# Kernel optimization log

Measured on AMD Instinct MI355X. Metric: run time of the kernel, lower is better.

Reference implementation:

```python
import jax, jax.numpy as jnp
import numpy as np

NBINS = (128, 64, 32)
LOG2PI = float(np.log(2.0 * np.pi))


def _quadratic_spline_stack(x, genes_oi, local_gene_ix, delta, uh, uw):
    """Stack of piecewise-quadratic (piecewise-linear density) splines on [0,1].
    Per split with n heights / n-1 widths (n-1 bins). Returns (outputs, logabsdet)."""
    uh_oi = uh[genes_oi]  # [G, sum(n)]
    uw_oi = uw[genes_oi]  # [G, sum(n-1)]
    outputs = x
    logabsdet = jnp.zeros_like(x)
    oh = ow = od = 0
    for n in NBINS:
        nh, nw = n, n - 1
        uhs = uh_oi[:, oh:oh + nh]
        uws = uw_oi[:, ow:ow + nw]
        ds = delta[:, od:od + nh]
        oh += nh; ow += nw; od += nh
        # per-gene bin widths / locations
        widths_g = jax.nn.softmax(uws, axis=-1)                     # [G, nw]
        bl = jnp.cumsum(widths_g, axis=-1)
        bl = bl.at[:, -1].set(1.0)
        bin_loc_g = jnp.pad(bl, ((0, 0), (1, 0)))                   # [G, nw+1]
        # gather per cut
        w = widths_g[local_gene_ix]                                 # [N, nw]
        loc = bin_loc_g[local_gene_ix]                              # [N, nw+1]
        # per-cut knot heights: gene baseline + cell/gene delta, normalized to unit area
        h_un = jnp.exp(uhs[local_gene_ix] + ds)                     # [N, nh]
        area = jnp.sum(0.5 * (h_un[:, :-1] + h_un[:, 1:]) * w, axis=-1, keepdims=True)
        h = h_un / area                                             # [N, nh]
        seg = 0.5 * (h[:, :-1] + h[:, 1:]) * w                      # bin masses [N, nw]
        left_cdf = jnp.pad(jnp.cumsum(seg, axis=-1)[:, :-1], ((0, 0), (1, 0)))  # [N, nw]
        # locate bin
        bin_idx = jnp.clip(jnp.sum(outputs[:, None] >= loc, axis=-1) - 1, 0, nw - 1)
        gi = bin_idx[:, None]
        loc_l = jnp.take_along_axis(loc, gi, -1)[:, 0]
        w_b = jnp.take_along_axis(w, gi, -1)[:, 0]
        cdf_l = jnp.take_along_axis(left_cdf, gi, -1)[:, 0]
        h_l = jnp.take_along_axis(h, gi, -1)[:, 0]
        h_r = jnp.take_along_axis(h, gi + 1, -1)[:, 0]
        alpha = (outputs - loc_l) / w_b
        outputs = (0.5 * (h_r - h_l) * w_b) * alpha * alpha + h_l * w_b * alpha + cdf_l
        logabsdet = logabsdet + jnp.log(h_l + (h_r - h_l) * alpha)
    return outputs, logabsdet


def setup_inputs() -> dict:
    key = jax.random.key(0)
    ks = jax.random.split(key, 10)
    B, L, G_total, G_oi, C, N = 512, 16, 20000, 500, 224, 200000
    clustering = jax.random.uniform(ks[0], (B, L), dtype=jnp.float32)
    coordinates = jax.random.uniform(ks[1], (N,), dtype=jnp.float32, minval=1e-4, maxval=1.0 - 1e-4)
    genes_oi = jax.random.randint(ks[2], (G_oi,), 0, G_total)
    local_gene_ix = jax.random.randint(ks[3], (N,), 0, G_oi)
    local_cellxgene_ix = jax.random.randint(ks[4], (N,), 0, B * G_oi)
    localcellxgene_ix = jax.random.randint(ks[5], (N,), 0, B * G_total)
    logit_weight = jax.random.normal(ks[6], (G_total, L, C), dtype=jnp.float32) * 0.01
    rho_weight = jax.random.normal(ks[7], (G_total, L), dtype=jnp.float32) * 0.05
    rho_bias = 1e-5 + (1.0 - 1e-5) * jax.random.uniform(ks[8], (G_total,), dtype=jnp.float32)
    k9, k10 = jax.random.split(ks[9])
    unnormalized_heights = jax.random.normal(k9, (G_total, sum(NBINS)), dtype=jnp.float32) * 0.1
    unnormalized_widths = jax.random.normal(k10, (G_total, sum(n - 1 for n in NBINS)), dtype=jnp.float32) * 0.1
    return dict(clustering=clustering, coordinates=coordinates, genes_oi=genes_oi,
                local_gene_ix=local_gene_ix, local_cellxgene_ix=local_cellxgene_ix,
                localcellxgene_ix=localcellxgene_ix, logit_weight=logit_weight,
                rho_weight=rho_weight, rho_bias=rho_bias,
                unnormalized_heights=unnormalized_heights,
                unnormalized_widths=unnormalized_widths)


def reference(clustering, coordinates, genes_oi, local_gene_ix, local_cellxgene_ix,
              localcellxgene_ix, logit_weight, rho_weight, rho_bias,
              unnormalized_heights, unnormalized_widths):
    B = clustering.shape[0]
    G = genes_oi.shape[0]
    n_total_genes = rho_bias.shape[0]
    # Decoder (n_layers=0 -> nn_output = latent)
    lw_oi = logit_weight[genes_oi]                                   # [G, L, C]
    mixture_delta = jnp.einsum('bl,glc->bgc', clustering, lw_oi)     # [B, G, C]
    rho_delta = clustering @ rho_weight.T                            # [B, G_total]
    rho = jax.nn.softmax(jnp.log(rho_bias)[None, :] + rho_delta, axis=-1)
    rho_cuts = rho.reshape(-1)[localcellxgene_ix]                    # [N]
    md_cuts = mixture_delta.reshape(B * G, -1)[local_cellxgene_ix]   # [N, C]
    _, lik_mixture = _quadratic_spline_stack(coordinates, genes_oi, local_gene_ix,
                                             md_cuts, unnormalized_heights, unnormalized_widths)
    lik_overall = jnp.log(rho_cuts) + jnp.log(jnp.float32(n_total_genes))
    elbo = -jnp.sum(lik_mixture + lik_overall)
    # Normal(0, exp(log_scale=0)=1) regularization log-probs
    def normal_logpdf(v):
        return -0.5 * v * v - 0.5 * LOG2PI
    elbo = elbo - jnp.sum(normal_logpdf(lw_oi))
    elbo = elbo - jnp.sum(normal_logpdf(rho_weight[genes_oi]))
    return elbo
```

## Files before the change

kernel.cpp:

```cpp
#include <hip/hip_runtime.h>
#include <cstddef>

#define LOG2PI_F 1.8378770664093453f

typedef float f2 __attribute__((ext_vector_type(2)));

__device__ __forceinline__ float wave_sum(float v) {
#pragma unroll
    for (int o = 32; o >= 1; o >>= 1) v += __shfl_xor(v, o, 64);
    return v;
}
__device__ __forceinline__ float wave_max(float v) {
#pragma unroll
    for (int o = 32; o >= 1; o >>= 1) v = fmaxf(v, __shfl_xor(v, o, 64));
    return v;
}
__device__ __forceinline__ float wave_scan_incl(float v, int lane) {
#pragma unroll
    for (int o = 1; o < 64; o <<= 1) {
        float t = __shfl_up(v, o, 64);
        if (lane >= o) v += t;
    }
    return v;
}

__device__ __forceinline__ float dot16(const f2* __restrict__ a, const f2* __restrict__ b) {
    f2 dv = a[0] * b[0];
#pragma unroll
    for (int l = 1; l < 8; ++l) dv = __builtin_elementwise_fma(a[l], b[l], dv);
    return dv.x + dv.y;
}

__global__ void k_prep_genes(const int* __restrict__ genes_oi,
                             const float* __restrict__ uh, const float* __restrict__ uw,
                             float4* __restrict__ pk, int* __restrict__ counts, int G_oi) {
    const int g = blockIdx.x;
    const int t = threadIdx.x;
    if (t == 0) counts[g] = 0;
    const int gs = genes_oi[g];
    const float* uhg = uh + (size_t)gs * 224;
    const float* uwg = uw + (size_t)gs * 221;

    const int NH[3] = {128, 64, 32};
    const int OH[3] = {0, 128, 192};
    const int OW[3] = {0, 127, 190};
    const int SO[3] = {0, 128, 191};
#pragma unroll
    for (int lev = 0; lev < 3; ++lev) {
        const int nw = NH[lev] - 1;
        float v0 = (t < nw)      ? uwg[OW[lev] + t]      : -INFINITY;
        float v1 = (t + 64 < nw) ? uwg[OW[lev] + t + 64] : -INFINITY;
        float mx = wave_max(fmaxf(v0, v1));
        float e0 = (t < nw)      ? __expf(v0 - mx) : 0.f;
        float e1 = (t + 64 < nw) ? __expf(v1 - mx) : 0.f;
        float inv = 1.0f / wave_sum(e0 + e1);
        float w0 = e0 * inv, w1 = e1 * inv;
        float i0 = wave_scan_incl(w0, t);
        float tot0 = __shfl(i0, 63, 64);
        float i1 = wave_scan_incl(w1, t) + tot0;
        if (t < nw) {
            float loc = (t == nw - 1) ? 1.0f : i0;
            pk[(size_t)(SO[lev] + t) * G_oi + g] = make_float4(uhg[OH[lev] + t + 1], 0.5f * w0, loc, 0.f);
        }
        if (t + 64 < nw) {
            int j = t + 64;
            float loc = (j == nw - 1) ? 1.0f : i1;
            pk[(size_t)(SO[lev] + j) * G_oi + g] = make_float4(uhg[OH[lev] + j + 1], 0.5f * w1, loc, 0.f);
        }
    }
    if (t == 0) pk[(size_t)127 * G_oi + g] = make_float4(uhg[0], uhg[128], uhg[192], 0.f);
}

__global__ void k_prep_lwT(const int* __restrict__ genes_oi,
                           const float* __restrict__ lw, const float* __restrict__ rw,
                           float* __restrict__ lwT, float* __restrict__ pB) {
    const int g = blockIdx.x;
    const int tid = threadIdx.x;
    const int gs = genes_oi[g];
    const float* src = lw + (size_t)gs * 3584;
    float* dst = lwT + (size_t)g * 3584;
    float acc = 0.f;
    if (tid < 224) {
        float vv[16];
#pragma unroll
        for (int l = 0; l < 16; ++l) {
            float v = src[l * 224 + tid];
            vv[l] = v;
            acc = fmaf(v, v, acc);
        }
        float4* d4 = (float4*)(dst + (size_t)tid * 16);
#pragma unroll
        for (int q = 0; q < 4; ++q)
            d4[q] = make_float4(vv[4 * q + 0], vv[4 * q + 1], vv[4 * q + 2], vv[4 * q + 3]);
    }
    if (tid < 16) { float v = rw[(size_t)gs * 16 + tid]; acc = fmaf(v, v, acc); }
    __shared__ float sm[256];
    sm[tid] = acc;
    __syncthreads();
    for (int o = 128; o > 0; o >>= 1) { if (tid < o) sm[tid] += sm[tid + o]; __syncthreads(); }
    if (tid == 0) pB[g] = 0.5f * sm[0] + 0.5f * LOG2PI_F * (3584.0f + 16.0f);
}

__global__ void k_hist_logrb(const int* __restrict__ lcx, int* __restrict__ counts,
                             const float* __restrict__ rho_bias, float* __restrict__ logrb,
                             int N, int G_oi, int G_total) {
    int i = blockIdx.x * blockDim.x + threadIdx.x;
    if (i < G_total) logrb[i] = __logf(rho_bias[i]);
    if (i < N) atomicAdd(&counts[(unsigned)lcx[i] % (unsigned)G_oi], 1);
}

__global__ void k_scan(const int* __restrict__ counts, int* __restrict__ offsets,
                       int* __restrict__ cursor, int G_oi) {
    __shared__ int sm[512];
    const int t = threadIdx.x;
    int v = (t < G_oi) ? counts[t] : 0;
    sm[t] = v;
    __syncthreads();
    for (int o = 1; o < 512; o <<= 1) {
        int add = (t >= o) ? sm[t - o] : 0;
        __syncthreads();
        sm[t] += add;
        __syncthreads();
    }
    if (t < G_oi) {
        offsets[t + 1] = sm[t];
        cursor[t] = sm[t] - v;
    }
    if (t == 0) offsets[0] = 0;
}

__global__ void k_scatter(const float* __restrict__ coord, const int* __restrict__ lgix,
                          const int* __restrict__ lcx, const int* __restrict__ lc2,
                          int* __restrict__ cursor, float4* __restrict__ xv, int N, int G_oi) {
    int i = blockIdx.x * blockDim.x + threadIdx.x;
    if (i >= N) return;
    unsigned v = (unsigned)lcx[i];
    unsigned g = v % (unsigned)G_oi;
    int pos = atomicAdd(&cursor[g], 1);
    int b1 = (int)(v / (unsigned)G_oi);
    xv[pos] = make_float4(coord[i], __int_as_float((b1 << 16) | lgix[i]),
                          __int_as_float(lc2[i]), 0.f);
}

__global__ void k_lse4(const float* __restrict__ clustering, const float* __restrict__ rw,
                       const float* __restrict__ logrb, float* __restrict__ lse,
                       int G_total, int B) {
    const int b0 = blockIdx.x * 4;
    const int tid = threadIdx.x;
    const int nc = min(4, B - b0);

    f2 cl[4][8];
#pragma unroll
    for (int c = 0; c < 4; ++c) {
        if (c < nc) {
            const float4* c4 = (const float4*)(clustering + (size_t)(b0 + c) * 16);
#pragma unroll
            for (int q = 0; q < 4; ++q) {
                float4 v = c4[q];
                cl[c][2 * q + 0] = (f2){v.x, v.y};
                cl[c][2 * q + 1] = (f2){v.z, v.w};
            }
        } else {
#pragma unroll
            for (int l = 0; l < 8; ++l) cl[c][l] = (f2){0.f, 0.f};
        }
    }

    float m[4], s[4];
#pragma unroll
    for (int c = 0; c < 4; ++c) { m[c] = -INFINITY; s[c] = 0.f; }

    for (int g = tid; g < G_total; g += 256) {
        const float4* r4 = (const float4*)(rw + (size_t)g * 16);
        f2 rv[8];
#pragma unroll
        for (int q = 0; q < 4; ++q) {
            float4 v = r4[q];
            rv[2 * q + 0] = (f2){v.x, v.y};
            rv[2 * q + 1] = (f2){v.z, v.w};
        }
        const float lb = logrb[g];
#pragma unroll
        for (int c = 0; c < 4; ++c) {
            float d = dot16(cl[c], rv);
            float logit = lb + d;
            float mn = fmaxf(m[c], logit);
            s[c] = s[c] * __expf(m[c] - mn) + __expf(logit - mn);
            m[c] = mn;
        }
    }

    __shared__ float ms[4][256], ss[4][256];
#pragma unroll
    for (int c = 0; c < 4; ++c) { ms[c][tid] = m[c]; ss[c][tid] = s[c]; }
    __syncthreads();
    for (int o = 128; o > 0; o >>= 1) {
        if (tid < o) {
#pragma unroll
            for (int c = 0; c < 4; ++c) {
                float m2 = ms[c][tid + o], s2 = ss[c][tid + o];
                float mn = fmaxf(ms[c][tid], m2);
                ss[c][tid] = ss[c][tid] * __expf(ms[c][tid] - mn) + s2 * __expf(m2 - mn);
                ms[c][tid] = mn;
            }
        }
        __syncthreads();
    }
    if (tid < 4 && tid < nc) lse[b0 + tid] = ms[tid][0] + __logf(ss[tid][0]);
}

__launch_bounds__(512, 4)
__global__ void k_main2(const float4* __restrict__ xv,
                        const int* __restrict__ offsets,
                        const float* __restrict__ clustering,
                        const float* __restrict__ lwT,
                        const float4* __restrict__ pk,
                        const float* __restrict__ rw,
                        const float* __restrict__ logrb,
                        const float* __restrict__ lse,
                        float* __restrict__ pA, int G_oi, int G_total) {
    const int g = blockIdx.x;
    const int tid = threadIdx.x;
    const float* lwg = lwT + (size_t)g * 3584;
    const int s = offsets[g], e = offsets[g + 1];
    const float logGt = __logf((float)G_total);
    float acc = 0.f;

    __shared__ int    s_cnt[512];
    __shared__ int    s_cur[512];
    __shared__ float4 s_v[512];
    __shared__ float  wsm[8];

    for (int base = s; base < e; base += 512) {
        const int cnt = min(512, e - base);
        const bool valid = tid < cnt;
        float4 v0 = xv[valid ? base + tid : s];
        const int gh_0 = __float_as_int(v0.y) & 0xffff;

        s_cnt[tid] = 0;
        __syncthreads();
        if (valid) atomicAdd(&s_cnt[gh_0], 1);
        __syncthreads();
        int v = s_cnt[tid];
        for (int o = 1; o < 512; o <<= 1) {
            int add = (tid >= o) ? s_cnt[tid - o] : 0;
            __syncthreads();
            s_cnt[tid] += add;
            __syncthreads();
        }
        s_cur[tid] = s_cnt[tid] - v;
        __syncthreads();
        if (valid) {
            int pos = atomicAdd(&s_cur[gh_0], 1);
            s_v[pos] = v0;
        }
        __syncthreads();

        if (valid) {
            float4 vv = s_v[tid];
            float x = vv.x;
            const int meta = __float_as_int(vv.y);
            const int gh  = meta & 0xffff;
            const int b1  = meta >> 16;
            const int lc2 = __float_as_int(vv.z);

            f2 cl[8];
            {
                const float4* c4 = (const float4*)(clustering + (size_t)b1 * 16);
#pragma unroll
                for (int q = 0; q < 4; ++q) {
                    float4 t4 = c4[q];
                    cl[2 * q + 0] = (f2){t4.x, t4.y};
                    cl[2 * q + 1] = (f2){t4.z, t4.w};
                }
            }
            const float4 uh0 = pk[(size_t)127 * G_oi + gh];
            const float uh0v[3] = {uh0.x, uh0.y, uh0.z};

            float lad = 0.f;
            const int NH[3] = {128, 64, 32};
            const int OH[3] = {0, 128, 192};
            const int SO[3] = {0, 128, 191};
#pragma unroll
            for (int lev = 0; lev < 3; ++lev) {
                const int nw = NH[lev] - 1;
                const float* rowbase = lwg + (size_t)OH[lev] * 16;
                float hp = __expf(uh0v[lev] + dot16((const f2*)rowbase, cl));
                float h_l = hp, h_r = hp, whb = 0.f, loc_l = 0.f, cdf = 0.f, area = 0.f;
                int in = 0;
                const float4* pks = pk + (size_t)SO[lev] * G_oi + gh;
                for (int j = 0; j < nw; ++j) {
                    const f2* row = (const f2*)(rowbase + (size_t)(j + 1) * 16);
                    float d = dot16(row, cl);
                    float4 pkv = *pks;
                    pks += G_oi;
                    float hn = __expf(pkv.x + d);
                    float seg = (hp + hn) * pkv.y;
                    bool inJ = (in == j);
                    if (inJ) { h_r = hn; whb = pkv.y; }
                    bool adv = (x >= pkv.z) && (j < nw - 1);
                    if (adv) { cdf += seg; h_l = hn; loc_l = pkv.z; in = j + 1; }
                    area += seg;
                    hp = hn;
                }
                float inv_area = __builtin_amdgcn_rcpf(area);
                float alpha = (x - loc_l) * 0.5f * __builtin_amdgcn_rcpf(whb);
                float t2 = whb * alpha;
                x = (t2 * fmaf(h_r - h_l, alpha, 2.f * h_l) + cdf) * inv_area;
                lad += __logf(fmaf(h_r - h_l, alpha, h_l)) - __logf(area);
            }

            unsigned b2 = (unsigned)lc2 / (unsigned)G_total;
            unsigned gt = (unsigned)lc2 - b2 * (unsigned)G_total;
            f2 c2[8], r2[8];
            {
                const float4* c24 = (const float4*)(clustering + (size_t)b2 * 16);
                const float4* r4  = (const float4*)(rw + (size_t)gt * 16);
#pragma unroll
                for (int q = 0; q < 4; ++q) {
                    float4 a = c24[q], b = r4[q];
                    c2[2 * q + 0] = (f2){a.x, a.y}; c2[2 * q + 1] = (f2){a.z, a.w};
                    r2[2 * q + 0] = (f2){b.x, b.y}; r2[2 * q + 1] = (f2){b.z, b.w};
                }
            }
            float d2 = dot16(c2, r2);
            float lik = logrb[gt] + d2 - lse[b2] + logGt;
            acc -= (lad + lik);
        }
    }

    acc = wave_sum(acc);
    if ((tid & 63) == 0) wsm[tid >> 6] = acc;
    __syncthreads();
    if (tid == 0) {
        float t = 0.f;
#pragma unroll
        for (int w = 0; w < 8; ++w) t += wsm[w];
        pA[g] = t;
    }
}

__global__ void k_final(const float* __restrict__ pA, const float* __restrict__ pB,
                        float* __restrict__ out, int nA, int nB) {
    const int tid = threadIdx.x;
    float acc = 0.f;
    for (int i = tid; i < nA; i += blockDim.x) acc += pA[i];
    for (int i = tid; i < nB; i += blockDim.x) acc += pB[i];
    __shared__ float sm[256];
    sm[tid] = acc;
    __syncthreads();
    for (int o = 128; o > 0; o >>= 1) { if (tid < o) sm[tid] += sm[tid + o]; __syncthreads(); }
    if (tid == 0) out[0] = sm[0];
}

extern "C" void kernel_launch(void* const* d_in, const int* in_sizes, int n_in,
                              void* d_out, int out_size, void* d_ws, size_t ws_size,
                              hipStream_t stream) {
    const float* clustering        = (const float*)d_in[0];
    const float* coordinates       = (const float*)d_in[1];
    const int*   genes_oi          = (const int*)d_in[2];
    const int*   local_gene_ix     = (const int*)d_in[3];
    const int*   local_cellxgene_ix= (const int*)d_in[4];
    const int*   localcellxgene_ix = (const int*)d_in[5];
    const float* lw                = (const float*)d_in[6];
    const float* rw                = (const float*)d_in[7];
    const float* rho_bias          = (const float*)d_in[8];
    const float* uh                = (const float*)d_in[9];
    const float* uw                = (const float*)d_in[10];

    const int G_total = in_sizes[8];
    const int G_oi    = in_sizes[2];
    const int N       = in_sizes[1];
    const int L       = in_sizes[7] / G_total;
    const int B       = in_sizes[0] / L;

    size_t off = 0;
    char* base = (char*)d_ws;
    auto alloc = [&](size_t nbytes) {
        char* p = base + off;
        off = (off + nbytes + 15) & ~(size_t)15;
        return (void*)p;
    };
    float*  pA      = (float*)alloc(sizeof(float) * (G_oi + 16));
    float*  pB      = (float*)alloc(sizeof(float) * (G_oi + 16));
    float*  lse     = (float*)alloc(sizeof(float) * (B + 16));
    float*  logrb   = (float*)alloc(sizeof(float) * G_total);
    float*  lwT     = (float*)alloc(sizeof(float) * (size_t)G_oi * 3584);
    float4* pk      = (float4*)alloc(sizeof(float4) * (size_t)G_oi * 224);
    int*    counts  = (int*)alloc(sizeof(int) * 512);
    int*    offsets = (int*)alloc(sizeof(int) * 512);
    int*    cursor  = (int*)alloc(sizeof(int) * 512);
    float4* xv      = (float4*)alloc(sizeof(float4) * (size_t)N);
    (void)ws_size;

    const int TPB = 256;
    k_prep_genes<<<G_oi, 64, 0, stream>>>(genes_oi, uh, uw, pk, counts, G_oi);
    k_prep_lwT<<<G_oi, 256, 0, stream>>>(genes_oi, lw, rw, lwT, pB);
    k_hist_logrb<<<(N + TPB - 1) / TPB, TPB, 0, stream>>>(local_cellxgene_ix, counts,
                                                          rho_bias, logrb, N, G_oi, G_total);
    k_scan<<<1, 512, 0, stream>>>(counts, offsets, cursor, G_oi);
    k_scatter<<<(N + TPB - 1) / TPB, TPB, 0, stream>>>(coordinates, local_gene_ix,
                                                       local_cellxgene_ix, localcellxgene_ix,
                                                       cursor, xv, N, G_oi);
    k_lse4<<<(B + 3) / 4, 256, 0, stream>>>(clustering, rw, logrb, lse, G_total, B);
    k_main2<<<G_oi, 512, 0, stream>>>(xv, offsets, clustering, lwT, pk,
                                      rw, logrb, lse, pA, G_oi, G_total);
    k_final<<<1, 256, 0, stream>>>(pA, pB, (float*)d_out, G_oi, G_oi);
}
```

Measured before the change: 633.4 us.

## Fuse gene prep kernels, split LSE over more blocks, unroll spline bin loop

Merges the two per-gene prep kernels into one launch, so the spline table and transposed logit weights are built by the same block. The softmax-normalizer kernel now handles two cells per block instead of four and processes two genes per thread per iteration, giving more blocks and more loads in flight. The main kernel's bin loop is unrolled by four with the table loads and dot products hoisted ahead of the sequential update chain. This removes one launch and exposes more memory-level parallelism, at the cost of more register pressure in the main kernel. The remainder block assumes nw-1 is a multiple of 4 plus 3, which holds for bin counts 127, 63 and 31.

```diff
diff --git a/kernel.cpp b/kernel.cpp
--- a/kernel.cpp
+++ b/kernel.cpp
@@ -31,49 +31,11 @@
     return dv.x + dv.y;
 }
 
-__global__ void k_prep_genes(const int* __restrict__ genes_oi,
+__global__ void k_prep_fused(const int* __restrict__ genes_oi,
+                             const float* __restrict__ lw, const float* __restrict__ rw,
                              const float* __restrict__ uh, const float* __restrict__ uw,
+                             float* __restrict__ lwT, float* __restrict__ pB,
                              float4* __restrict__ pk, int* __restrict__ counts, int G_oi) {
-    const int g = blockIdx.x;
-    const int t = threadIdx.x;
-    if (t == 0) counts[g] = 0;
-    const int gs = genes_oi[g];
-    const float* uhg = uh + (size_t)gs * 224;
-    const float* uwg = uw + (size_t)gs * 221;
-
-    const int NH[3] = {128, 64, 32};
-    const int OH[3] = {0, 128, 192};
-    const int OW[3] = {0, 127, 190};
-    const int SO[3] = {0, 128, 191};
-#pragma unroll
-    for (int lev = 0; lev < 3; ++lev) {
-        const int nw = NH[lev] - 1;
-        float v0 = (t < nw)      ? uwg[OW[lev] + t]      : -INFINITY;
-        float v1 = (t + 64 < nw) ? uwg[OW[lev] + t + 64] : -INFINITY;
-        float mx = wave_max(fmaxf(v0, v1));
-        float e0 = (t < nw)      ? __expf(v0 - mx) : 0.f;
-        float e1 = (t + 64 < nw) ? __expf(v1 - mx) : 0.f;
-        float inv = 1.0f / wave_sum(e0 + e1);
-        float w0 = e0 * inv, w1 = e1 * inv;
-        float i0 = wave_scan_incl(w0, t);
-        float tot0 = __shfl(i0, 63, 64);
-        float i1 = wave_scan_incl(w1, t) + tot0;
-        if (t < nw) {
-            float loc = (t == nw - 1) ? 1.0f : i0;
-            pk[(size_t)(SO[lev] + t) * G_oi + g] = make_float4(uhg[OH[lev] + t + 1], 0.5f * w0, loc, 0.f);
-        }
-        if (t + 64 < nw) {
-            int j = t + 64;
-            float loc = (j == nw - 1) ? 1.0f : i1;
-            pk[(size_t)(SO[lev] + j) * G_oi + g] = make_float4(uhg[OH[lev] + j + 1], 0.5f * w1, loc, 0.f);
-        }
-    }
-    if (t == 0) pk[(size_t)127 * G_oi + g] = make_float4(uhg[0], uhg[128], uhg[192], 0.f);
-}
-
-__global__ void k_prep_lwT(const int* __restrict__ genes_oi,
-                           const float* __restrict__ lw, const float* __restrict__ rw,
-                           float* __restrict__ lwT, float* __restrict__ pB) {
     const int g = blockIdx.x;
     const int tid = threadIdx.x;
     const int gs = genes_oi[g];
@@ -98,7 +60,44 @@
     sm[tid] = acc;
     __syncthreads();
     for (int o = 128; o > 0; o >>= 1) { if (tid < o) sm[tid] += sm[tid + o]; __syncthreads(); }
-    if (tid == 0) pB[g] = 0.5f * sm[0] + 0.5f * LOG2PI_F * (3584.0f + 16.0f);
+    if (tid == 0) {
+        pB[g] = 0.5f * sm[0] + 0.5f * LOG2PI_F * (3584.0f + 16.0f);
+        counts[g] = 0;
+    }
+
+    if (tid < 64) {
+        const int t = tid;
+        const float* uhg = uh + (size_t)gs * 224;
+        const float* uwg = uw + (size_t)gs * 221;
+        const int NH[3] = {128, 64, 32};
+        const int OH[3] = {0, 128, 192};
+        const int OW[3] = {0, 127, 190};
+        const int SO[3] = {0, 128, 191};
+#pragma unroll
+        for (int lev = 0; lev < 3; ++lev) {
+            const int nw = NH[lev] - 1;
+            float v0 = (t < nw)      ? uwg[OW[lev] + t]      : -INFINITY;
+            float v1 = (t + 64 < nw) ? uwg[OW[lev] + t + 64] : -INFINITY;
+            float mx = wave_max(fmaxf(v0, v1));
+            float e0 = (t < nw)      ? __expf(v0 - mx) : 0.f;
+            float e1 = (t + 64 < nw) ? __expf(v1 - mx) : 0.f;
+            float inv = 1.0f / wave_sum(e0 + e1);
+            float w0 = e0 * inv, w1 = e1 * inv;
+            float i0 = wave_scan_incl(w0, t);
+            float tot0 = __shfl(i0, 63, 64);
+            float i1 = wave_scan_incl(w1, t) + tot0;
+            if (t < nw) {
+                float loc = (t == nw - 1) ? 1.0f : i0;
+                pk[(size_t)(SO[lev] + t) * G_oi + g] = make_float4(uhg[OH[lev] + t + 1], 0.5f * w0, loc, 0.f);
+            }
+            if (t + 64 < nw) {
+                int j = t + 64;
+                float loc = (j == nw - 1) ? 1.0f : i1;
+                pk[(size_t)(SO[lev] + j) * G_oi + g] = make_float4(uhg[OH[lev] + j + 1], 0.5f * w1, loc, 0.f);
+            }
+        }
+        if (t == 0) pk[(size_t)127 * G_oi + g] = make_float4(uhg[0], uhg[128], uhg[192], 0.f);
+    }
 }
 
 __global__ void k_hist_logrb(const int* __restrict__ lcx, int* __restrict__ counts,
@@ -142,16 +141,16 @@
                           __int_as_float(lc2[i]), 0.f);
 }
 
-__global__ void k_lse4(const float* __restrict__ clustering, const float* __restrict__ rw,
+__global__ void k_lse2(const float* __restrict__ clustering, const float* __restrict__ rw,
                        const float* __restrict__ logrb, float* __restrict__ lse,
                        int G_total, int B) {
-    const int b0 = blockIdx.x * 4;
+    const int b0 = blockIdx.x * 2;
     const int tid = threadIdx.x;
-    const int nc = min(4, B - b0);
-
-    f2 cl[4][8];
-#pragma unroll
-    for (int c = 0; c < 4; ++c) {
+    const int nc = min(2, B - b0);
+
+    f2 cl[2][8];
+#pragma unroll
+    for (int c = 0; c < 2; ++c) {
         if (c < nc) {
             const float4* c4 = (const float4*)(clustering + (size_t)(b0 + c) * 16);
 #pragma unroll
@@ -166,38 +165,60 @@
         }
     }
 
-    float m[4], s[4];
-#pragma unroll
-    for (int c = 0; c < 4; ++c) { m[c] = -INFINITY; s[c] = 0.f; }
-
-    for (int g = tid; g < G_total; g += 256) {
+    float m[2], s[2];
+#pragma unroll
+    for (int c = 0; c < 2; ++c) { m[c] = -INFINITY; s[c] = 0.f; }
+
+    for (int g = tid; g < G_total; g += 512) {
+        const int g2 = g + 256;
+        const bool has2 = g2 < G_total;
         const float4* r4 = (const float4*)(rw + (size_t)g * 16);
+        const float4* r4b = (const float4*)(rw + (size_t)(has2 ? g2 : g) * 16);
+        float4 ra[4], rb[4];
+#pragma unroll
+        for (int q = 0; q < 4; ++q) { ra[q] = r4[q]; rb[q] = r4b[q]; }
+        const float lb  = logrb[g];
+        const float lb2 = logrb[has2 ? g2 : g];
+
         f2 rv[8];
 #pragma unroll
         for (int q = 0; q < 4; ++q) {
-            float4 v = r4[q];
-            rv[2 * q + 0] = (f2){v.x, v.y};
-            rv[2 * q + 1] = (f2){v.z, v.w};
-        }
-        const float lb = logrb[g];
-#pragma unroll
-        for (int c = 0; c < 4; ++c) {
+            rv[2 * q + 0] = (f2){ra[q].x, ra[q].y};
+            rv[2 * q + 1] = (f2){ra[q].z, ra[q].w};
+        }
+#pragma unroll
+        for (int c = 0; c < 2; ++c) {
             float d = dot16(cl[c], rv);
             float logit = lb + d;
             float mn = fmaxf(m[c], logit);
             s[c] = s[c] * __expf(m[c] - mn) + __expf(logit - mn);
             m[c] = mn;
         }
-    }
-
-    __shared__ float ms[4][256], ss[4][256];
-#pragma unroll
-    for (int c = 0; c < 4; ++c) { ms[c][tid] = m[c]; ss[c][tid] = s[c]; }
+        if (has2) {
+#pragma unroll
+            for (int q = 0; q < 4; ++q) {
+                rv[2 * q + 0] = (f2){rb[q].x, rb[q].y};
+                rv[2 * q + 1] = (f2){rb[q].z, rb[q].w};
+            }
+#pragma unroll
+            for (int c = 0; c < 2; ++c) {
+                float d = dot16(cl[c], rv);
+                float logit = lb2 + d;
+                float mn = fmaxf(m[c], logit);
+                s[c] = s[c] * __expf(m[c] - mn) + __expf(logit - mn);
+                m[c] = mn;
+            }
+        }
+    }
+
+    __shared__ float ms[2][256], ss[2][256];
+#pragma unroll
+    for (int c = 0; c < 2; ++c) { ms[c][tid] = m[c]; ss[c][tid] = s[c]; }
     __syncthreads();
     for (int o = 128; o > 0; o >>= 1) {
         if (tid < o) {
 #pragma unroll
-            for (int c = 0; c < 4; ++c) {
+            for (int c = 0; c < 2; ++c) {
                 float m2 = ms[c][tid + o], s2 = ss[c][tid + o];
                 float mn = fmaxf(ms[c][tid], m2);
                 ss[c][tid] = ss[c][tid] * __expf(ms[c][tid] - mn) + s2 * __expf(m2 - mn);
@@ -206,7 +227,7 @@
         }
         __syncthreads();
     }
-    if (tid < 4 && tid < nc) lse[b0 + tid] = ms[tid][0] + __logf(ss[tid][0]);
+    if (tid < 2 && tid < nc) lse[b0 + tid] = ms[tid][0] + __logf(ss[tid][0]);
 }
 
 __launch_bounds__(512, 4)
@@ -289,20 +310,45 @@
                 float h_l = hp, h_r = hp, whb = 0.f, loc_l = 0.f, cdf = 0.f, area = 0.f;
                 int in = 0;
                 const float4* pks = pk + (size_t)SO[lev] * G_oi + gh;
-                for (int j = 0; j < nw; ++j) {
-                    const f2* row = (const f2*)(rowbase + (size_t)(j + 1) * 16);
-                    float d = dot16(row, cl);
-                    float4 pkv = *pks;
-                    pks += G_oi;
+
+                auto STEP = [&](int j, float4 pkv, float d) {
                     float hn = __expf(pkv.x + d);
                     float seg = (hp + hn) * pkv.y;
-                    bool inJ = (in == j);
-                    if (inJ) { h_r = hn; whb = pkv.y; }
+                    if (in == j) { h_r = hn; whb = pkv.y; }
                     bool adv = (x >= pkv.z) && (j < nw - 1);
                     if (adv) { cdf += seg; h_l = hn; loc_l = pkv.z; in = j + 1; }
                     area += seg;
                     hp = hn;
+                };
+
+                int j = 0;
+                for (; j + 3 < nw; j += 4) {
+                    float4 q0 = pks[0];
+                    float4 q1 = pks[(size_t)G_oi];
+                    float4 q2 = pks[(size_t)2 * G_oi];
+                    float4 q3 = pks[(size_t)3 * G_oi];
+                    pks += (size_t)4 * G_oi;
+                    float d0 = dot16((const f2*)(rowbase + (size_t)(j + 1) * 16), cl);
+                    float d1 = dot16((const f2*)(rowbase + (size_t)(j + 2) * 16), cl);
+                    float d2 = dot16((const f2*)(rowbase + (size_t)(j + 3) * 16), cl);
+                    float d3 = dot16((const f2*)(rowbase + (size_t)(j + 4) * 16), cl);
+                    STEP(j + 0, q0, d0);
+                    STEP(j + 1, q1, d1);
+                    STEP(j + 2, q2, d2);
+                    STEP(j + 3, q3, d3);
                 }
+                {
+                    float4 q0 = pks[0];
+                    float4 q1 = pks[(size_t)G_oi];
+                    float4 q2 = pks[(size_t)2 * G_oi];
+                    float d0 = dot16((const f2*)(rowbase + (size_t)(j + 1) * 16), cl);
+                    float d1 = dot16((const f2*)(rowbase + (size_t)(j + 2) * 16), cl);
+                    float d2 = dot16((const f2*)(rowbase + (size_t)(j + 3) * 16), cl);
+                    STEP(j + 0, q0, d0);
+                    STEP(j + 1, q1, d1);
+                    STEP(j + 2, q2, d2);
+                }
+
                 float inv_area = __builtin_amdgcn_rcpf(area);
                 float alpha = (x - loc_l) * 0.5f * __builtin_amdgcn_rcpf(whb);
                 float t2 = whb * alpha;
@@ -323,8 +369,8 @@
                     r2[2 * q + 0] = (f2){b.x, b.y}; r2[2 * q + 1] = (f2){b.z, b.w};
                 }
             }
-            float d2 = dot16(c2, r2);
-            float lik = logrb[gt] + d2 - lse[b2] + logGt;
+            float d2v = dot16(c2, r2);
+            float lik = logrb[gt] + d2v - lse[b2] + logGt;
             acc -= (lad + lik);
         }
     }
@@ -394,15 +440,14 @@
     (void)ws_size;
 
     const int TPB = 256;
-    k_prep_genes<<<G_oi, 64, 0, stream>>>(genes_oi, uh, uw, pk, counts, G_oi);
-    k_prep_lwT<<<G_oi, 256, 0, stream>>>(genes_oi, lw, rw, lwT, pB);
+    k_prep_fused<<<G_oi, 256, 0, stream>>>(genes_oi, lw, rw, uh, uw, lwT, pB, pk, counts, G_oi);
     k_hist_logrb<<<(N + TPB - 1) / TPB, TPB, 0, stream>>>(local_cellxgene_ix, counts,
                                                           rho_bias, logrb, N, G_oi, G_total);
     k_scan<<<1, 512, 0, stream>>>(counts, offsets, cursor, G_oi);
     k_scatter<<<(N + TPB - 1) / TPB, TPB, 0, stream>>>(coordinates, local_gene_ix,
                                                        local_cellxgene_ix, localcellxgene_ix,
                                                        cursor, xv, N, G_oi);
-    k_lse4<<<(B + 3) / 4, 256, 0, stream>>>(clustering, rw, logrb, lse, G_total, B);
+    k_lse2<<<(B + 1) / 2, 256, 0, stream>>>(clustering, rw, logrb, lse, G_total, B);
     k_main2<<<G_oi, 512, 0, stream>>>(xv, offsets, clustering, lwT, pk,
                                       rw, logrb, lse, pA, G_oi, G_total);
     k_final<<<1, 256, 0, stream>>>(pA, pB, (float*)d_out, G_oi, G_oi);
```

Result: faster. 599.4 us (-5.4%).
